# Performance work log

Hardware: AMD Instinct MI355X
Metric: run time of the kernel (lower is better)

## Reference

```python
import jax, jax.numpy as jnp
import numpy as np
import math

B, P, N, DM, H, DK, DH, DF = 2, 12, 170, 64, 8, 8, 32, 256
SQ = math.sqrt(DK)

def _ln(x, g, b):
    m = jnp.mean(x, -1, keepdims=True)
    v = jnp.var(x, -1, keepdims=True)
    return (x - m) / jnp.sqrt(v + 1e-5) * g + b

def _nozero_softmax(s):
    # faithful to nozero_softmax: mask = (s != 0), max over full row, +1e-5 in denom
    mask = (s != 0).astype(s.dtype)
    e = jnp.exp(s - jnp.max(s, -1, keepdims=True)) * mask
    return e / (jnp.sum(e, -1, keepdims=True) + 1e-5)

def _meta(c, w1, b1, w2, b2):
    # MetaLearner: [B,P,N,DM] -> [3,B,P,N,H,DK,DM]
    h = jax.nn.relu(c @ w1 + b1) @ w2 + b2
    h = h.reshape(c.shape[:3] + (3, H, DK, DM))
    return jnp.moveaxis(h, 3, 0)

def _mhlin(W, x):
    # multihead_linear_transform: per-position meta weight applied to x
    return jnp.einsum('bpnhkd,bpnd->bpnhk', W, x)

def _gdc(data, W1, W2):
    # Gated_Dynamic_Connection (noGC=False). data: [G,B,P,N,C]
    d = jnp.moveaxis(data, 0, 3)  # [B,P,N,G,C]
    a = jnp.einsum('bpngc,gcd->bpngd', d, W1)
    s = jax.nn.softmax(jax.nn.relu(jnp.einsum('bpngc,gcd->bpngd', d, W2)), axis=3)
    return jnp.sum(a * s, axis=3)  # [B,P,N,DM]

def _swish_gate(x, out, wg, bg, wo, bo):
    h = (x @ wg + bg) * out
    return (h * jax.nn.sigmoid(h)) @ wo + bo

def _spatial(Q, K, V, T):
    # adjacency-masked spatial attention. Dense-masked form is exactly the
    # scatter-into-zeros buffer of the original: zero where T==0, QK/sqrt(dk) on edges.
    s = jnp.einsum('bpihk,bpjhk->bphij', Q, K) / SQ
    Tb = T if T.ndim == 2 else T[:, :, None]  # adaptive graph [B,P,1,N,N]
    s = s * (Tb != 0)
    alpha = _nozero_softmax(s) * Tb
    return jnp.einsum('bphij,bpjhk->hbpik', alpha, V)  # [H,B,P,N,DK]

def _temporal(Q, K, V):
    s = jnp.einsum('bqnhk,bpnhk->bnhqp', Q, K) / SQ
    alpha = jax.nn.softmax(s, -1)
    return jnp.einsum('bnhqp,bpnhk->hbqnk', alpha, V)  # [H,B,P,N,DK]

def _retnet(Q, K, V, D):
    # multihead_temporal_regnet with g=1 leading dim folded in
    r = jnp.einsum('bqnhk,bpnhk->bnhqp', Q, K) / SQ
    r = r * D  # D: [H,P,P] causal decay
    rs = jnp.maximum(jnp.abs(jnp.sum(r, -1, keepdims=True)), 1.0)
    r = r / rs
    return jnp.einsum('bnhqp,bpnhk->hbqnk', r, V)  # [H,B,P,N,DK]

def _forward(x, c_x, enc, T, A, D, mr_w1, mr_b1, mr_w2, mr_b2, ms0_w1, ms0_b1, ms0_w2, ms0_b2, ms1_w1, ms1_b1, ms1_w2, ms1_b2, gr_W1, gr_W2, gs0_W1, gs0_W2, gs1_W1, gs1_W2, g2_W1, g2_W2, ge_W1, ge_W2, swr_wg, swr_bg, swr_wo, swr_bo, sws_wg, sws_bg, sws_wo, sws_bo, swe_wg, swe_bg, swe_wo, swe_bo, lnr_g, lnr_b, lns_g, lns_b, lne_g, lne_b, lnf_g, lnf_b, wq, wk, wv, f_w1, f_b1, f_w2, f_b2):
    # 1) RetNet-style temporal self retention (meta-learned QKV)
    W = _meta(c_x, mr_w1, mr_b1, mr_w2, mr_b2)
    o = _gdc(_retnet(_mhlin(W[0], x), _mhlin(W[1], x), _mhlin(W[2], x), D), gr_W1, gr_W2)
    o = _swish_gate(x, o, swr_wg, swr_bg, swr_wo, swr_bo)
    x1 = _ln(o + x, lnr_g, lnr_b)
    # 2) Spatial self attention: predefined graph + adaptive graph branches
    W0 = _meta(c_x, ms0_w1, ms0_b1, ms0_w2, ms0_b2)
    o0 = _gdc(_spatial(_mhlin(W0[0], x1), _mhlin(W0[1], x1), _mhlin(W0[2], x1), T), gs0_W1, gs0_W2)
    W1m = _meta(c_x, ms1_w1, ms1_b1, ms1_w2, ms1_b2)
    o1 = _gdc(_spatial(_mhlin(W1m[0], x1), _mhlin(W1m[1], x1), _mhlin(W1m[2], x1), A), gs1_W1, gs1_W2)
    o = _gdc(jnp.stack([o0, o1], 0), g2_W1, g2_W2)
    o = _swish_gate(x1, o, sws_wg, sws_bg, sws_wo, sws_bo)
    x2 = _ln(o + x1, lns_g, lns_b)
    # 3) Temporal encoder-decoder attention
    q = (x2 @ wq).reshape(B, P, N, H, DK)
    k = (enc @ wk).reshape(B, P, N, H, DK)
    v = (enc @ wv).reshape(B, P, N, H, DK)
    o = _gdc(_temporal(q, k, v), ge_W1, ge_W2)
    o = _swish_gate(x2, o, swe_wg, swe_bg, swe_wo, swe_bo)
    x3 = _ln(o + x2, lne_g, lne_b)
    # 4) FFN
    o = jax.nn.relu(x3 @ f_w1 + f_b1) @ f_w2 + f_b2
    return _ln(o + x3, lnf_g, lnf_b)


def setup_inputs() -> dict:
    key = jax.random.key(0)
    ks = iter(jax.random.split(key, 100))
    def rn(shape, s=0.05):
        return (jax.random.normal(next(ks), shape) * s).astype(jnp.float32)
    inp = {}
    inp['x'] = jax.random.normal(next(ks), (B, P, N, DM), jnp.float32)
    inp['c_x'] = jax.random.normal(next(ks), (B, P, N, DM), jnp.float32)
    inp['enc'] = jax.random.normal(next(ks), (B, P, N, DM), jnp.float32)
    mT = jax.random.uniform(next(ks), (N, N)) < 0.1
    inp['T'] = (jax.random.uniform(next(ks), (N, N)) * mT).astype(jnp.float32)
    mA = jax.random.uniform(next(ks), (B, P, N, N)) < 0.05
    inp['A'] = (jax.random.uniform(next(ks), (B, P, N, N)) * mA).astype(jnp.float32)
    q = np.arange(P)
    gam = 1.0 - 2.0 ** (-5.0 - np.arange(H))
    Dm = np.where(q[:, None] >= q[None, :], gam[:, None, None] ** (q[:, None] - q[None, :]), 0.0)
    inp['D'] = jnp.asarray(Dm, jnp.float32)  # [H,P,P]
    for p in ['mr', 'ms0', 'ms1']:
        inp[p + '_w1'] = rn((DM, DH)); inp[p + '_b1'] = jnp.zeros((DH,), jnp.float32)
        inp[p + '_w2'] = rn((DH, 3 * H * DK * DM)); inp[p + '_b2'] = jnp.zeros((3 * H * DK * DM,), jnp.float32)
    for p in ['gr', 'gs0', 'gs1', 'ge']:
        inp[p + '_W1'] = rn((H, DK, DM)); inp[p + '_W2'] = rn((H, DK, DM))
    inp['g2_W1'] = rn((2, DM, DM)); inp['g2_W2'] = rn((2, DM, DM))
    for p in ['swr', 'sws', 'swe']:
        inp[p + '_wg'] = rn((DM, DM)); inp[p + '_bg'] = jnp.zeros((DM,), jnp.float32)
        inp[p + '_wo'] = rn((DM, DM)); inp[p + '_bo'] = jnp.zeros((DM,), jnp.float32)
    for p in ['lnr', 'lns', 'lne', 'lnf']:
        inp[p + '_g'] = jnp.ones((DM,), jnp.float32); inp[p + '_b'] = jnp.zeros((DM,), jnp.float32)
    inp['wq'] = rn((DM, DM)); inp['wk'] = rn((DM, DM)); inp['wv'] = rn((DM, DM))
    inp['f_w1'] = rn((DM, DF)); inp['f_b1'] = jnp.zeros((DF,), jnp.float32)
    inp['f_w2'] = rn((DF, DM)); inp['f_b2'] = jnp.zeros((DM,), jnp.float32)
    return inp


def reference(x, c_x, enc, T, A, D, mr_w1, mr_b1, mr_w2, mr_b2, ms0_w1, ms0_b1, ms0_w2, ms0_b2, ms1_w1, ms1_b1, ms1_w2, ms1_b2, gr_W1, gr_W2, gs0_W1, gs0_W2, gs1_W1, gs1_W2, g2_W1, g2_W2, ge_W1, ge_W2, swr_wg, swr_bg, swr_wo, swr_bo, sws_wg, sws_bg, sws_wo, sws_bo, swe_wg, swe_bg, swe_wo, swe_bo, lnr_g, lnr_b, lns_g, lns_b, lne_g, lne_b, lnf_g, lnf_b, wq, wk, wv, f_w1, f_b1, f_w2, f_b2):
    return _forward(x, c_x, enc, T, A, D, mr_w1, mr_b1, mr_w2, mr_b2, ms0_w1, ms0_b1, ms0_w2, ms0_b2, ms1_w1, ms1_b1, ms1_w2, ms1_b2, gr_W1, gr_W2, gs0_W1, gs0_W2, gs1_W1, gs1_W2, g2_W1, g2_W2, ge_W1, ge_W2, swr_wg, swr_bg, swr_wo, swr_bo, sws_wg, sws_bg, sws_wo, sws_bo, swe_wg, swe_bg, swe_wo, swe_bo, lnr_g, lnr_b, lns_g, lns_b, lne_g, lne_b, lnf_g, lnf_b, wq, wk, wv, f_w1, f_b1, f_w2, f_b2)
```

## Files before the change

kernel.cpp:

```cpp
#include <hip/hip_runtime.h>
#include <hip/hip_bf16.h>
#include <math.h>

namespace {

constexpr int B_ = 2, P_ = 12, N_ = 170, DM_ = 64, H_ = 8, DK_ = 8, DH_ = 32, DF_ = 256;
constexpr int T_ = B_ * P_ * N_;
constexpr float SQRT_DK = 2.8284271247461903f;

constexpr int NG_ = 12;
constexpr int NC_ = 66;
constexpr int WFRAG_G = NG_ * NC_ * 64 * 8;

typedef __attribute__((ext_vector_type(4))) short short4v;
typedef __attribute__((ext_vector_type(8))) short short8v;
typedef __attribute__((ext_vector_type(4))) float float4v;

__device__ __forceinline__ unsigned short f2bf(float x) {
    union { float f; unsigned int u; } c; c.f = x;
    unsigned int r = (c.u + 0x7FFFu + ((c.u >> 16) & 1u)) >> 16;
    return (unsigned short)r;
}

__global__ void k_hr3(const float* __restrict__ c_x,
                      const float* __restrict__ w1a, const float* __restrict__ b1a,
                      const float* __restrict__ w1b, const float* __restrict__ b1b,
                      const float* __restrict__ w1c, const float* __restrict__ b1c,
                      float* __restrict__ hra, float* __restrict__ hrb,
                      float* __restrict__ hrc) {
    int z = blockIdx.y;
    const float* w1 = z == 0 ? w1a : (z == 1 ? w1b : w1c);
    const float* b1 = z == 0 ? b1a : (z == 1 ? b1b : b1c);
    float* hr = z == 0 ? hra : (z == 1 ? hrb : hrc);
    int idx = blockIdx.x * 256 + threadIdx.x;
    if (idx >= T_ * DH_) return;
    int t = idx / DH_, j = idx % DH_;
    float acc = b1[j];
    const float* cx = c_x + t * DM_;
    #pragma unroll
    for (int d = 0; d < DM_; ++d) acc += cx[d] * w1[d * DH_ + j];
    hr[idx] = fmaxf(acc, 0.f);
}

__global__ void k_wconv(const float* __restrict__ w2a, const float* __restrict__ b2a,
                        const float* __restrict__ w2b, const float* __restrict__ b2b,
                        const float* __restrict__ w2c, const float* __restrict__ b2c,
                        unsigned short* __restrict__ Wfrag) {
    int idx = blockIdx.x * 256 + threadIdx.x;
    if (idx >= 3 * NG_ * NC_ * 64) return;
    int lane = idx & 63;
    int c = (idx >> 6) % NC_;
    int ng = (idx >> 6) / NC_ % NG_;
    int g = idx / (64 * NC_ * NG_);
    const float* w2 = g == 0 ? w2a : (g == 1 ? w2b : w2c);
    const float* b2 = g == 0 ? b2a : (g == 1 ? b2b : b2c);
    int m = ng * 16 + (lane & 15);
    int u = c >> 1;
    int d0 = (c & 1) * 32 + (lane >> 4) * 8;
    const float* src = (u < DH_) ? (w2 + u * 12288 + m * 64 + d0) : (b2 + m * 64 + d0);
    short8v o;
    #pragma unroll
    for (int j = 0; j < 8; ++j) o[j] = (short)f2bf(src[j]);
    *(short8v*)(Wfrag + (size_t)idx * 8) = o;
}

__global__ __launch_bounds__(256) void k_meta_gemm2(
    const float* __restrict__ hr0, const float* __restrict__ hr1,
    const float* __restrict__ xin,
    const unsigned short* __restrict__ Wf0, const unsigned short* __restrict__ Wf1,
    float* __restrict__ out0, float* __restrict__ out1) {
    const int bz = blockIdx.z;
    const float* hr = bz ? hr1 : hr0;
    const unsigned short* Wf = bz ? Wf1 : Wf0;
    float* out = bz ? out1 : out0;

    const int tid = threadIdx.x;
    const int wv = tid >> 6, lane = tid & 63;
    const int l15 = lane & 15, quad = lane >> 4;
    const int g16 = blockIdx.x * 4 + wv;
    if (g16 >= 255) return;
    const int t = g16 * 16 + l15;
    const int nb = blockIdx.y;

    const float* xp = xin + t * 64 + quad * 8;
    float4v xa = *(const float4v*)(xp);
    float4v xb = *(const float4v*)(xp + 4);
    float4v xc = *(const float4v*)(xp + 32);
    float4v xd = *(const float4v*)(xp + 36);
    float xr[16] = {xa.x, xa.y, xa.z, xa.w, xb.x, xb.y, xb.z, xb.w,
                    xc.x, xc.y, xc.z, xc.w, xd.x, xd.y, xd.z, xd.w};

    const float* hrp = hr + t * 32;
    float4v acc[4] = {{0.f,0.f,0.f,0.f},{0.f,0.f,0.f,0.f},
                      {0.f,0.f,0.f,0.f},{0.f,0.f,0.f,0.f}};

    const unsigned short* wb = Wf + ((size_t)(nb * 4) * NC_ * 64 + lane) * 8;
    const size_t qstride = (size_t)NC_ * 64 * 8;
    const size_t cstride = 64 * 8;

    for (int u = 0; u < 33; ++u) {
        float hrv = (u < DH_) ? hrp[u] : 1.0f;
        short8v a0, a1;
        #pragma unroll
        for (int j = 0; j < 8; ++j) {
            a0[j] = (short)f2bf(hrv * xr[j]);
            a1[j] = (short)f2bf(hrv * xr[8 + j]);
        }
        const unsigned short* wc = wb + (size_t)(2 * u) * cstride;
        #pragma unroll
        for (int q = 0; q < 4; ++q) {
            short8v b0 = *(const short8v*)(wc + q * qstride);
            short8v b1 = *(const short8v*)(wc + q * qstride + cstride);
            acc[q] = __builtin_amdgcn_mfma_f32_16x16x32_bf16(a0, b0, acc[q], 0, 0, 0);
            acc[q] = __builtin_amdgcn_mfma_f32_16x16x32_bf16(a1, b1, acc[q], 0, 0, 0);
        }
    }

    #pragma unroll
    for (int q = 0; q < 4; ++q) {
        #pragma unroll
        for (int r = 0; r < 4; ++r) {
            int tt = g16 * 16 + quad * 4 + r;
            out[tt * 192 + nb * 64 + q * 16 + l15] = acc[q][r];
        }
    }
}

__global__ __launch_bounds__(256) void k_retnet(const float* __restrict__ qkv,
                                                const float* __restrict__ Dm,
                                                float* __restrict__ att) {
    const int bn = blockIdx.x;
    const int b = bn / N_, n = bn % N_;
    __shared__ float S[12][192];
    __shared__ float Ds[8 * 145];
    const int tid = threadIdx.x;
    for (int e = tid; e < 12 * 192; e += 256) {
        int p = e / 192, c = e % 192;
        S[p][c] = qkv[((size_t)((b * P_ + p) * N_ + n)) * 192 + c];
    }
    for (int e = tid; e < 1152; e += 256) {
        Ds[(e / 144) * 145 + (e % 144)] = Dm[e];
    }
    __syncthreads();
    const int qq = tid >> 6;
    const int lane = tid & 63;
    const int h = lane >> 3, k = lane & 7;
    for (int q = qq; q < P_; q += 4) {
        float Qv = S[q][h * 8 + k];
        float r[P_];
        float rsum = 0.f;
        #pragma unroll
        for (int p = 0; p < P_; ++p) {
            float prod = Qv * S[p][64 + h * 8 + k];
            prod += __shfl_xor(prod, 1, 64);
            prod += __shfl_xor(prod, 2, 64);
            prod += __shfl_xor(prod, 4, 64);
            float s = (prod / SQRT_DK) * Ds[h * 145 + q * 12 + p];
            r[p] = s; rsum += s;
        }
        float rs = fmaxf(fabsf(rsum), 1.0f);
        float acc = 0.f;
        #pragma unroll
        for (int p = 0; p < P_; ++p) acc += (r[p] / rs) * S[p][128 + h * 8 + k];
        att[((size_t)((b * P_ + q) * N_ + n)) * 64 + lane] = acc;
    }
}

__global__ __launch_bounds__(256) void k_temporal(const float* __restrict__ qkv,
                                                  float* __restrict__ att) {
    const int bn = blockIdx.x;
    const int b = bn / N_, n = bn % N_;
    __shared__ float S[12][192];
    const int tid = threadIdx.x;
    for (int e = tid; e < 12 * 192; e += 256) {
        int p = e / 192, c = e % 192;
        S[p][c] = qkv[((size_t)((b * P_ + p) * N_ + n)) * 192 + c];
    }
    __syncthreads();
    const int qq = tid >> 6;
    const int lane = tid & 63;
    const int h = lane >> 3, k = lane & 7;
    for (int q = qq; q < P_; q += 4) {
        float Qv = S[q][h * 8 + k];
        float s[P_];
        float mx = -1e30f;
        #pragma unroll
        for (int p = 0; p < P_; ++p) {
            float prod = Qv * S[p][64 + h * 8 + k];
            prod += __shfl_xor(prod, 1, 64);
            prod += __shfl_xor(prod, 2, 64);
            prod += __shfl_xor(prod, 4, 64);
            float v = prod / SQRT_DK;
            s[p] = v; mx = fmaxf(mx, v);
        }
        float den = 0.f, acc = 0.f;
        #pragma unroll
        for (int p = 0; p < P_; ++p) {
            float e = expf(s[p] - mx);
            den += e;
            acc += e * S[p][128 + h * 8 + k];
        }
        att[((size_t)((b * P_ + q) * N_ + n)) * 64 + lane] = acc / den;
    }
}

__global__ __launch_bounds__(256) void k_spatial_sparse(
    const float* __restrict__ qkvA, const float* __restrict__ qkvB,
    const float* __restrict__ Tm, const float* __restrict__ Am,
    float* __restrict__ attA, float* __restrict__ attB) {
    const int bp = blockIdx.y;
    const int g = blockIdx.z;
    const float* qkv = g ? qkvB : qkvA;
    float* att = g ? attB : attA;

    __shared__ int2 elist[4][176];

    const int tid = threadIdx.x;
    const int wv = tid >> 6, lane = tid & 63;
    const int i = blockIdx.x * 4 + wv;
    if (i >= N_) return;

    int2* el = elist[wv];
    const float* Trow = g ? (Am + (size_t)(bp * N_ + i) * N_) : (Tm + (size_t)i * N_);
    int nnz = 0;
    #pragma unroll
    for (int c = 0; c < 3; ++c) {
        int j = c * 64 + lane;
        float w = (j < N_) ? Trow[j] : 0.f;
        unsigned long long m = __ballot(w != 0.f);
        if (w != 0.f) {
            int pos = nnz + (int)__popcll(m & ((1ull << lane) - 1ull));
            el[pos] = make_int2(j, __float_as_int(w));
        }
        nnz += (int)__popcll(m);
    }

    const float q = qkv[(size_t)(bp * N_ + i) * 192 + lane];
    float m = 0.f;
    float den = 0.f, acc = 0.f;
    int e = 0;
    for (; e + 1 < nnz; e += 2) {
        int2 e0 = el[e], e1 = el[e + 1];
        const float* r0 = qkv + (size_t)(bp * N_ + e0.x) * 192;
        const float* r1 = qkv + (size_t)(bp * N_ + e1.x) * 192;
        float k0 = r0[64 + lane], v0 = r0[128 + lane];
        float k1 = r1[64 + lane], v1 = r1[128 + lane];
        float p0 = q * k0, p1 = q * k1;
        p0 += __shfl_xor(p0, 1, 64); p1 += __shfl_xor(p1, 1, 64);
        p0 += __shfl_xor(p0, 2, 64); p1 += __shfl_xor(p1, 2, 64);
        p0 += __shfl_xor(p0, 4, 64); p1 += __shfl_xor(p1, 4, 64);
        float s0 = p0 / SQRT_DK, s1 = p1 / SQRT_DK;
        float mn = fmaxf(m, fmaxf(s0, s1));
        float cs = expf(m - mn);
        float x0 = (s0 != 0.f) ? expf(s0 - mn) : 0.f;
        float x1 = (s1 != 0.f) ? expf(s1 - mn) : 0.f;
        den = den * cs + x0 + x1;
        acc = acc * cs + x0 * __int_as_float(e0.y) * v0
                       + x1 * __int_as_float(e1.y) * v1;
        m = mn;
    }
    if (e < nnz) {
        int2 e0 = el[e];
        const float* r0 = qkv + (size_t)(bp * N_ + e0.x) * 192;
        float k0 = r0[64 + lane], v0 = r0[128 + lane];
        float p0 = q * k0;
        p0 += __shfl_xor(p0, 1, 64);
        p0 += __shfl_xor(p0, 2, 64);
        p0 += __shfl_xor(p0, 4, 64);
        float s0 = p0 / SQRT_DK;
        float mn = fmaxf(m, s0);
        float cs = expf(m - mn);
        float x0 = (s0 != 0.f) ? expf(s0 - mn) : 0.f;
        den = den * cs + x0;
        acc = acc * cs + x0 * __int_as_float(e0.y) * v0;
    }

    att[(size_t)(bp * N_ + i) * 64 + lane] = acc / (den + 1e-5f);
}

__device__ __forceinline__ float gdc8(const float* dv, const float* W1,
                                      const float* W2, int dm) {
    float a[8], s[8];
    #pragma unroll
    for (int g = 0; g < 8; ++g) {
        float aa = 0.f, ss = 0.f;
        #pragma unroll
        for (int c = 0; c < 8; ++c) {
            float d = dv[g * 8 + c];
            aa += d * W1[(g * 8 + c) * 64 + dm];
            ss += d * W2[(g * 8 + c) * 64 + dm];
        }
        a[g] = aa; s[g] = fmaxf(ss, 0.f);
    }
    float mx = s[0];
    #pragma unroll
    for (int g = 1; g < 8; ++g) mx = fmaxf(mx, s[g]);
    float den = 0.f, o = 0.f;
    #pragma unroll
    for (int g = 0; g < 8; ++g) { float e = expf(s[g] - mx); den += e; o += a[g] * e; }
    return o / den;
}

__device__ __forceinline__ float ln_out(float r, int dm, const float* g, const float* b) {
    float m = r, m2 = r * r;
    #pragma unroll
    for (int off = 32; off; off >>= 1) { m += __shfl_xor(m, off, 64); m2 += __shfl_xor(m2, off, 64); }
    m *= (1.f / 64.f); m2 *= (1.f / 64.f);
    float var = m2 - m * m;
    return (r - m) * rsqrtf(var + 1e-5f) * g[dm] + b[dm];
}

__global__ __launch_bounds__(64) void k_gsl(const float* __restrict__ att, const float* __restrict__ xin,
    const float* W1, const float* W2,
    const float* wg, const float* bg,
    const float* wo, const float* bo,
    const float* lng, const float* lnb, float* __restrict__ xout) {
    int t = blockIdx.x, dm = threadIdx.x;
    __shared__ float dv[64], xv[64], swv[64];
    dv[dm] = att[t * 64 + dm];
    xv[dm] = xin[t * 64 + dm];
    __syncthreads();
    float o = gdc8(dv, W1, W2, dm);
    float hg = bg[dm];
    #pragma unroll
    for (int d = 0; d < 64; ++d) hg += xv[d] * wg[d * 64 + dm];
    hg *= o;
    swv[dm] = hg / (1.f + expf(-hg));
    __syncthreads();
    float ov = bo[dm];
    #pragma unroll
    for (int d = 0; d < 64; ++d) ov += swv[d] * wo[d * 64 + dm];
    float r = ov + xv[dm];
    xout[t * 64 + dm] = ln_out(r, dm, lng, lnb);
}

__global__ __launch_bounds__(64) void k_spatial_fuse(
    const float* __restrict__ att0, const float* __restrict__ att1, const float* __restrict__ x1,
    const float* gs0_W1, const float* gs0_W2,
    const float* gs1_W1, const float* gs1_W2,
    const float* g2_W1, const float* g2_W2,
    const float* wg, const float* bg,
    const float* wo, const float* bo,
    const float* lng, const float* lnb, float* __restrict__ xout) {
    int t = blockIdx.x, dm = threadIdx.x;
    __shared__ float d0[64], d1[64], o0s[64], o1s[64], xv[64], swv[64];
    d0[dm] = att0[t * 64 + dm];
    d1[dm] = att1[t * 64 + dm];
    xv[dm] = x1[t * 64 + dm];
    __syncthreads();
    o0s[dm] = gdc8(d0, gs0_W1, gs0_W2, dm);
    o1s[dm] = gdc8(d1, gs1_W1, gs1_W2, dm);
    __syncthreads();
    float a0 = 0.f, s0 = 0.f, a1 = 0.f, s1 = 0.f;
    #pragma unroll
    for (int c = 0; c < 64; ++c) {
        a0 += o0s[c] * g2_W1[c * 64 + dm];
        s0 += o0s[c] * g2_W2[c * 64 + dm];
        a1 += o1s[c] * g2_W1[(64 + c) * 64 + dm];
        s1 += o1s[c] * g2_W2[(64 + c) * 64 + dm];
    }
    s0 = fmaxf(s0, 0.f); s1 = fmaxf(s1, 0.f);
    float mx = fmaxf(s0, s1);
    float e0 = expf(s0 - mx), e1 = expf(s1 - mx);
    float o = (a0 * e0 + a1 * e1) / (e0 + e1);
    float hg = bg[dm];
    #pragma unroll
    for (int d = 0; d < 64; ++d) hg += xv[d] * wg[d * 64 + dm];
    hg *= o;
    swv[dm] = hg / (1.f + expf(-hg));
    __syncthreads();
    float ov = bo[dm];
    #pragma unroll
    for (int d = 0; d < 64; ++d) ov += swv[d] * wo[d * 64 + dm];
    float r = ov + xv[dm];
    xout[t * 64 + dm] = ln_out(r, dm, lng, lnb);
}

__global__ __launch_bounds__(64) void k_qkvproj(const float* __restrict__ x2,
    const float* __restrict__ enc,
    const float* wq, const float* wk, const float* wv,
    float* __restrict__ qkv) {
    int t = blockIdx.x, dm = threadIdx.x;
    __shared__ float xv[64], ev[64];
    xv[dm] = x2[t * 64 + dm];
    ev[dm] = enc[t * 64 + dm];
    __syncthreads();
    float aq = 0.f, ak = 0.f, av = 0.f;
    #pragma unroll
    for (int d = 0; d < 64; ++d) {
        aq += xv[d] * wq[d * 64 + dm];
        ak += ev[d] * wk[d * 64 + dm];
        av += ev[d] * wv[d * 64 + dm];
    }
    qkv[t * 192 + dm] = aq;
    qkv[t * 192 + 64 + dm] = ak;
    qkv[t * 192 + 128 + dm] = av;
}

__global__ __launch_bounds__(64) void k_ffn(const float* __restrict__ x3,
    const float* w1, const float* b1,
    const float* w2, const float* b2,
    const float* lng, const float* lnb,
    float* __restrict__ out) {
    int t = blockIdx.x, dm = threadIdx.x;
    __shared__ float xv[64], hv[256];
    xv[dm] = x3[t * 64 + dm];
    __syncthreads();
    #pragma unroll
    for (int e = 0; e < 4; ++e) {
        int j = e * 64 + dm;
        float a = b1[j];
        #pragma unroll
        for (int d = 0; d < 64; ++d) a += xv[d] * w1[d * 256 + j];
        hv[j] = fmaxf(a, 0.f);
    }
    __syncthreads();
    float a = b2[dm];
    for (int j = 0; j < 256; ++j) a += hv[j] * w2[j * 64 + dm];
    float r = a + xv[dm];
    out[t * 64 + dm] = ln_out(r, dm, lng, lnb);
}

}

extern "C" void kernel_launch(void* const* d_in, const int* in_sizes, int n_in,
                              void* d_out, int out_size, void* d_ws, size_t ws_size,
                              hipStream_t stream) {
    (void)in_sizes; (void)n_in; (void)out_size; (void)ws_size;
    const float* x    = (const float*)d_in[0];
    const float* c_x  = (const float*)d_in[1];
    const float* enc  = (const float*)d_in[2];
    const float* Tm   = (const float*)d_in[3];
    const float* Am   = (const float*)d_in[4];
    const float* Dm   = (const float*)d_in[5];
    const float* mr_w1 = (const float*)d_in[6];
    const float* mr_b1 = (const float*)d_in[7];
    const float* mr_w2 = (const float*)d_in[8];
    const float* mr_b2 = (const float*)d_in[9];
    const float* ms0_w1 = (const float*)d_in[10];
    const float* ms0_b1 = (const float*)d_in[11];
    const float* ms0_w2 = (const float*)d_in[12];
    const float* ms0_b2 = (const float*)d_in[13];
    const float* ms1_w1 = (const float*)d_in[14];
    const float* ms1_b1 = (const float*)d_in[15];
    const float* ms1_w2 = (const float*)d_in[16];
    const float* ms1_b2 = (const float*)d_in[17];
    const float* gr_W1 = (const float*)d_in[18];
    const float* gr_W2 = (const float*)d_in[19];
    const float* gs0_W1 = (const float*)d_in[20];
    const float* gs0_W2 = (const float*)d_in[21];
    const float* gs1_W1 = (const float*)d_in[22];
    const float* gs1_W2 = (const float*)d_in[23];
    const float* g2_W1 = (const float*)d_in[24];
    const float* g2_W2 = (const float*)d_in[25];
    const float* ge_W1 = (const float*)d_in[26];
    const float* ge_W2 = (const float*)d_in[27];
    const float* swr_wg = (const float*)d_in[28];
    const float* swr_bg = (const float*)d_in[29];
    const float* swr_wo = (const float*)d_in[30];
    const float* swr_bo = (const float*)d_in[31];
    const float* sws_wg = (const float*)d_in[32];
    const float* sws_bg = (const float*)d_in[33];
    const float* sws_wo = (const float*)d_in[34];
    const float* sws_bo = (const float*)d_in[35];
    const float* swe_wg = (const float*)d_in[36];
    const float* swe_bg = (const float*)d_in[37];
    const float* swe_wo = (const float*)d_in[38];
    const float* swe_bo = (const float*)d_in[39];
    const float* lnr_g = (const float*)d_in[40];
    const float* lnr_b = (const float*)d_in[41];
    const float* lns_g = (const float*)d_in[42];
    const float* lns_b = (const float*)d_in[43];
    const float* lne_g = (const float*)d_in[44];
    const float* lne_b = (const float*)d_in[45];
    const float* lnf_g = (const float*)d_in[46];
    const float* lnf_b = (const float*)d_in[47];
    const float* wq = (const float*)d_in[48];
    const float* wk = (const float*)d_in[49];
    const float* wv = (const float*)d_in[50];
    const float* f_w1 = (const float*)d_in[51];
    const float* f_b1 = (const float*)d_in[52];
    const float* f_w2 = (const float*)d_in[53];
    const float* f_b2 = (const float*)d_in[54];

    float* ws   = (float*)d_ws;
    float* hr   = ws;
    float* hr2  = hr   + T_ * DH_;
    float* qkva = hr2  + T_ * DH_;
    float* qkvb = qkva + T_ * 192;
    float* atta = qkvb + T_ * 192;
    float* attb = atta + T_ * DM_;
    float* x1f  = attb + T_ * DM_;
    float* x2f  = x1f  + T_ * DM_;
    float* x3f  = x2f  + T_ * DM_;
    unsigned short* Wfrag = (unsigned short*)(x3f + T_ * DM_);
    float* hr_r = attb;

    k_wconv<<<(3 * NG_ * NC_ * 64 + 255) / 256, 256, 0, stream>>>(
        mr_w2, mr_b2, ms0_w2, ms0_b2, ms1_w2, ms1_b2, Wfrag);

    k_hr3<<<dim3(510, 3), 256, 0, stream>>>(c_x, mr_w1, mr_b1, ms0_w1, ms0_b1,
                                            ms1_w1, ms1_b1, hr_r, hr, hr2);

    k_meta_gemm2<<<dim3(64, 3, 1), 256, 0, stream>>>(
        hr_r, hr_r, x, Wfrag, Wfrag, qkva, qkva);
    k_retnet<<<B_ * N_, 256, 0, stream>>>(qkva, Dm, atta);
    k_gsl<<<T_, 64, 0, stream>>>(atta, x, gr_W1, gr_W2, swr_wg, swr_bg, swr_wo, swr_bo,
                                 lnr_g, lnr_b, x1f);

    k_meta_gemm2<<<dim3(64, 3, 2), 256, 0, stream>>>(
        hr, hr2, x1f, Wfrag + WFRAG_G, Wfrag + 2 * WFRAG_G, qkva, qkvb);
    k_spatial_sparse<<<dim3((N_ + 3) / 4, B_ * P_, 2), 256, 0, stream>>>(
        qkva, qkvb, Tm, Am, atta, attb);
    k_spatial_fuse<<<T_, 64, 0, stream>>>(atta, attb, x1f, gs0_W1, gs0_W2, gs1_W1, gs1_W2,
                                          g2_W1, g2_W2, sws_wg, sws_bg, sws_wo, sws_bo,
                                          lns_g, lns_b, x2f);

    k_qkvproj<<<T_, 64, 0, stream>>>(x2f, enc, wq, wk, wv, qkva);
    k_temporal<<<B_ * N_, 256, 0, stream>>>(qkva, atta);
    k_gsl<<<T_, 64, 0, stream>>>(atta, x2f, ge_W1, ge_W2, swe_wg, swe_bg, swe_wo, swe_bo,
                                 lne_g, lne_b, x3f);

    k_ffn<<<T_, 64, 0, stream>>>(x3f, f_w1, f_b1, f_w2, f_b2, lnf_g, lnf_b, (float*)d_out);
}
```

Baseline: 324.7 us.

## Fuse attention kernels with gated-dynamic-connection/swish/layernorm epilogues and merge prep kernels

Merges the weight conversion and hidden-layer prep kernels into one launch. Fuses retnet attention with its GDC/swish-gate/layernorm stage, spatial sparse attention (both graphs) with its fuse stage, and QKV projection plus temporal attention plus its gated stage into single kernels. The meta GEMM loop now loads hr as float4 and peels the bias step. This cuts launch count and intermediate global round-trips, but the fused epilogues run serialized per wave inside blocks with fewer blocks overall (340 for temporal/retnet), which may lower parallelism.

```diff
diff --git a/kernel.cpp b/kernel.cpp
--- a/kernel.cpp
+++ b/kernel.cpp
@@ -22,46 +22,46 @@
     return (unsigned short)r;
 }
 
-__global__ void k_hr3(const float* __restrict__ c_x,
+__global__ void k_pre(const float* __restrict__ c_x,
                       const float* __restrict__ w1a, const float* __restrict__ b1a,
                       const float* __restrict__ w1b, const float* __restrict__ b1b,
                       const float* __restrict__ w1c, const float* __restrict__ b1c,
+                      const float* __restrict__ w2a, const float* __restrict__ b2a,
+                      const float* __restrict__ w2b, const float* __restrict__ b2b,
+                      const float* __restrict__ w2c, const float* __restrict__ b2c,
                       float* __restrict__ hra, float* __restrict__ hrb,
-                      float* __restrict__ hrc) {
-    int z = blockIdx.y;
-    const float* w1 = z == 0 ? w1a : (z == 1 ? w1b : w1c);
-    const float* b1 = z == 0 ? b1a : (z == 1 ? b1b : b1c);
-    float* hr = z == 0 ? hra : (z == 1 ? hrb : hrc);
-    int idx = blockIdx.x * 256 + threadIdx.x;
-    if (idx >= T_ * DH_) return;
-    int t = idx / DH_, j = idx % DH_;
-    float acc = b1[j];
-    const float* cx = c_x + t * DM_;
-    #pragma unroll
-    for (int d = 0; d < DM_; ++d) acc += cx[d] * w1[d * DH_ + j];
-    hr[idx] = fmaxf(acc, 0.f);
-}
-
-__global__ void k_wconv(const float* __restrict__ w2a, const float* __restrict__ b2a,
-                        const float* __restrict__ w2b, const float* __restrict__ b2b,
-                        const float* __restrict__ w2c, const float* __restrict__ b2c,
-                        unsigned short* __restrict__ Wfrag) {
-    int idx = blockIdx.x * 256 + threadIdx.x;
-    if (idx >= 3 * NG_ * NC_ * 64) return;
-    int lane = idx & 63;
-    int c = (idx >> 6) % NC_;
-    int ng = (idx >> 6) / NC_ % NG_;
-    int g = idx / (64 * NC_ * NG_);
-    const float* w2 = g == 0 ? w2a : (g == 1 ? w2b : w2c);
-    const float* b2 = g == 0 ? b2a : (g == 1 ? b2b : b2c);
-    int m = ng * 16 + (lane & 15);
-    int u = c >> 1;
-    int d0 = (c & 1) * 32 + (lane >> 4) * 8;
-    const float* src = (u < DH_) ? (w2 + u * 12288 + m * 64 + d0) : (b2 + m * 64 + d0);
-    short8v o;
-    #pragma unroll
-    for (int j = 0; j < 8; ++j) o[j] = (short)f2bf(src[j]);
-    *(short8v*)(Wfrag + (size_t)idx * 8) = o;
+                      float* __restrict__ hrc, unsigned short* __restrict__ Wfrag) {
+    if (blockIdx.y == 0) {
+        int idx = blockIdx.x * 256 + threadIdx.x;
+        if (idx >= 3 * NG_ * NC_ * 64) return;
+        int lane = idx & 63;
+        int c = (idx >> 6) % NC_;
+        int ng = (idx >> 6) / NC_ % NG_;
+        int g = idx / (64 * NC_ * NG_);
+        const float* w2 = g == 0 ? w2a : (g == 1 ? w2b : w2c);
+        const float* b2 = g == 0 ? b2a : (g == 1 ? b2b : b2c);
+        int m = ng * 16 + (lane & 15);
+        int u = c >> 1;
+        int d0 = (c & 1) * 32 + (lane >> 4) * 8;
+        const float* src = (u < DH_) ? (w2 + u * 12288 + m * 64 + d0) : (b2 + m * 64 + d0);
+        short8v o;
+        #pragma unroll
+        for (int j = 0; j < 8; ++j) o[j] = (short)f2bf(src[j]);
+        *(short8v*)(Wfrag + (size_t)idx * 8) = o;
+    } else {
+        int z = blockIdx.y - 1;
+        const float* w1 = z == 0 ? w1a : (z == 1 ? w1b : w1c);
+        const float* b1 = z == 0 ? b1a : (z == 1 ? b1b : b1c);
+        float* hr = z == 0 ? hra : (z == 1 ? hrb : hrc);
+        int idx = blockIdx.x * 256 + threadIdx.x;
+        if (idx >= T_ * DH_) return;
+        int t = idx / DH_, j = idx % DH_;
+        float acc = b1[j];
+        const float* cx = c_x + t * DM_;
+        #pragma unroll
+        for (int d = 0; d < DM_; ++d) acc += cx[d] * w1[d * DH_ + j];
+        hr[idx] = fmaxf(acc, 0.f);
+    }
 }
 
 __global__ __launch_bounds__(256) void k_meta_gemm2(
@@ -98,15 +98,37 @@
     const size_t qstride = (size_t)NC_ * 64 * 8;
     const size_t cstride = 64 * 8;
 
-    for (int u = 0; u < 33; ++u) {
-        float hrv = (u < DH_) ? hrp[u] : 1.0f;
+    #pragma unroll 1
+    for (int u0 = 0; u0 < 32; u0 += 4) {
+        float4v h4 = *(const float4v*)(hrp + u0);
+        float hv4[4] = {h4.x, h4.y, h4.z, h4.w};
+        #pragma unroll
+        for (int du = 0; du < 4; ++du) {
+            float hrv = hv4[du];
+            short8v a0, a1;
+            #pragma unroll
+            for (int j = 0; j < 8; ++j) {
+                a0[j] = (short)f2bf(hrv * xr[j]);
+                a1[j] = (short)f2bf(hrv * xr[8 + j]);
+            }
+            const unsigned short* wc = wb + (size_t)(2 * (u0 + du)) * cstride;
+            #pragma unroll
+            for (int q = 0; q < 4; ++q) {
+                short8v b0 = *(const short8v*)(wc + q * qstride);
+                short8v b1 = *(const short8v*)(wc + q * qstride + cstride);
+                acc[q] = __builtin_amdgcn_mfma_f32_16x16x32_bf16(a0, b0, acc[q], 0, 0, 0);
+                acc[q] = __builtin_amdgcn_mfma_f32_16x16x32_bf16(a1, b1, acc[q], 0, 0, 0);
+            }
+        }
+    }
+    {
         short8v a0, a1;
         #pragma unroll
         for (int j = 0; j < 8; ++j) {
-            a0[j] = (short)f2bf(hrv * xr[j]);
-            a1[j] = (short)f2bf(hrv * xr[8 + j]);
-        }
-        const unsigned short* wc = wb + (size_t)(2 * u) * cstride;
+            a0[j] = (short)f2bf(xr[j]);
+            a1[j] = (short)f2bf(xr[8 + j]);
+        }
+        const unsigned short* wc = wb + (size_t)64 * cstride;
         #pragma unroll
         for (int q = 0; q < 4; ++q) {
             short8v b0 = *(const short8v*)(wc + q * qstride);
@@ -126,13 +148,50 @@
     }
 }
 
-__global__ __launch_bounds__(256) void k_retnet(const float* __restrict__ qkv,
-                                                const float* __restrict__ Dm,
-                                                float* __restrict__ att) {
+__device__ __forceinline__ float gdc8(const float* dv, const float* W1,
+                                      const float* W2, int dm) {
+    float a[8], s[8];
+    #pragma unroll
+    for (int g = 0; g < 8; ++g) {
+        float aa = 0.f, ss = 0.f;
+        #pragma unroll
+        for (int c = 0; c < 8; ++c) {
+            float d = dv[g * 8 + c];
+            aa += d * W1[(g * 8 + c) * 64 + dm];
+            ss += d * W2[(g * 8 + c) * 64 + dm];
+        }
+        a[g] = aa; s[g] = fmaxf(ss, 0.f);
+    }
+    float mx = s[0];
+    #pragma unroll
+    for (int g = 1; g < 8; ++g) mx = fmaxf(mx, s[g]);
+    float den = 0.f, o = 0.f;
+    #pragma unroll
+    for (int g = 0; g < 8; ++g) { float e = expf(s[g] - mx); den += e; o += a[g] * e; }
+    return o / den;
+}
+
+__device__ __forceinline__ float ln_out(float r, int dm, const float* g, const float* b) {
+    float m = r, m2 = r * r;
+    #pragma unroll
+    for (int off = 32; off; off >>= 1) { m += __shfl_xor(m, off, 64); m2 += __shfl_xor(m2, off, 64); }
+    m *= (1.f / 64.f); m2 *= (1.f / 64.f);
+    float var = m2 - m * m;
+    return (r - m) * rsqrtf(var + 1e-5f) * g[dm] + b[dm];
+}
+
+__global__ __launch_bounds__(256) void k_retnet_gsl(
+    const float* __restrict__ qkv, const float* __restrict__ Dm,
+    const float* __restrict__ xin,
+    const float* W1, const float* W2,
+    const float* wg, const float* bg, const float* wo, const float* bo,
+    const float* lng, const float* lnb,
+    float* __restrict__ x1f) {
     const int bn = blockIdx.x;
     const int b = bn / N_, n = bn % N_;
     __shared__ float S[12][192];
     __shared__ float Ds[8 * 145];
+    __shared__ float dvr[4][64], xvr[4][64], swb[4][64];
     const int tid = threadIdx.x;
     for (int e = tid; e < 12 * 192; e += 256) {
         int p = e / 192, c = e % 192;
@@ -142,10 +201,10 @@
         Ds[(e / 144) * 145 + (e % 144)] = Dm[e];
     }
     __syncthreads();
-    const int qq = tid >> 6;
+    const int wv = tid >> 6;
     const int lane = tid & 63;
     const int h = lane >> 3, k = lane & 7;
-    for (int q = qq; q < P_; q += 4) {
+    for (int q = wv; q < P_; q += 4) {
         float Qv = S[q][h * 8 + k];
         float r[P_];
         float rsum = 0.f;
@@ -162,25 +221,64 @@
         float acc = 0.f;
         #pragma unroll
         for (int p = 0; p < P_; ++p) acc += (r[p] / rs) * S[p][128 + h * 8 + k];
-        att[((size_t)((b * P_ + q) * N_ + n)) * 64 + lane] = acc;
-    }
-}
-
-__global__ __launch_bounds__(256) void k_temporal(const float* __restrict__ qkv,
-                                                  float* __restrict__ att) {
+
+        const size_t t64 = (size_t)((b * P_ + q) * N_ + n) * 64;
+        dvr[wv][lane] = acc;
+        xvr[wv][lane] = xin[t64 + lane];
+        __syncthreads();
+        float o = gdc8(dvr[wv], W1, W2, lane);
+        float hg = bg[lane];
+        #pragma unroll
+        for (int d = 0; d < 64; ++d) hg += xvr[wv][d] * wg[d * 64 + lane];
+        hg *= o;
+        swb[wv][lane] = hg / (1.f + expf(-hg));
+        __syncthreads();
+        float ov = bo[lane];
+        #pragma unroll
+        for (int d = 0; d < 64; ++d) ov += swb[wv][d] * wo[d * 64 + lane];
+        float rr = ov + xvr[wv][lane];
+        x1f[t64 + lane] = ln_out(rr, lane, lng, lnb);
+        __syncthreads();
+    }
+}
+
+__global__ __launch_bounds__(256) void k_temporal_full(
+    const float* __restrict__ x2f, const float* __restrict__ enc,
+    const float* __restrict__ wqm, const float* __restrict__ wkm,
+    const float* __restrict__ wvm,
+    const float* W1, const float* W2,
+    const float* wg, const float* bg, const float* wo, const float* bo,
+    const float* lng, const float* lnb,
+    float* __restrict__ x3f) {
     const int bn = blockIdx.x;
     const int b = bn / N_, n = bn % N_;
+    __shared__ float Sx[12][64], Se[12][64];
     __shared__ float S[12][192];
+    __shared__ float dvr[4][64], swb[4][64];
     const int tid = threadIdx.x;
-    for (int e = tid; e < 12 * 192; e += 256) {
-        int p = e / 192, c = e % 192;
-        S[p][c] = qkv[((size_t)((b * P_ + p) * N_ + n)) * 192 + c];
-    }
-    __syncthreads();
-    const int qq = tid >> 6;
+    for (int e = tid; e < 768; e += 256) {
+        int p = e >> 6, c = e & 63;
+        size_t t64 = (size_t)((b * P_ + p) * N_ + n) * 64;
+        Sx[p][c] = x2f[t64 + c];
+        Se[p][c] = enc[t64 + c];
+    }
+    __syncthreads();
+    #pragma unroll
+    for (int it = 0; it < 9; ++it) {
+        int e = it * 256 + tid;
+        int p = e / 192, j = e % 192;
+        const float* src = (j < 64) ? Sx[p] : Se[p];
+        const float* wm = (j < 64) ? (wqm + j) : (j < 128 ? (wkm + j - 64) : (wvm + j - 128));
+        float a = 0.f;
+        #pragma unroll
+        for (int d = 0; d < 64; ++d) a += src[d] * wm[d * 64];
+        S[p][j] = a;
+    }
+    __syncthreads();
+    const int wv = tid >> 6;
     const int lane = tid & 63;
     const int h = lane >> 3, k = lane & 7;
-    for (int q = qq; q < P_; q += 4) {
+    for (int q = wv; q < P_; q += 4) {
         float Qv = S[q][h * 8 + k];
         float s[P_];
         float mx = -1e30f;
@@ -200,201 +298,142 @@
             den += e;
             acc += e * S[p][128 + h * 8 + k];
         }
-        att[((size_t)((b * P_ + q) * N_ + n)) * 64 + lane] = acc / den;
-    }
-}
-
-__global__ __launch_bounds__(256) void k_spatial_sparse(
+        const size_t t64 = (size_t)((b * P_ + q) * N_ + n) * 64;
+        dvr[wv][lane] = acc / den;
+        __syncthreads();
+        float o = gdc8(dvr[wv], W1, W2, lane);
+        float hg = bg[lane];
+        #pragma unroll
+        for (int d = 0; d < 64; ++d) hg += Sx[q][d] * wg[d * 64 + lane];
+        hg *= o;
+        swb[wv][lane] = hg / (1.f + expf(-hg));
+        __syncthreads();
+        float ov = bo[lane];
+        #pragma unroll
+        for (int d = 0; d < 64; ++d) ov += swb[wv][d] * wo[d * 64 + lane];
+        float rr = ov + Sx[q][lane];
+        x3f[t64 + lane] = ln_out(rr, lane, lng, lnb);
+        __syncthreads();
+    }
+}
+
+__global__ __launch_bounds__(256) void k_spatial_all(
     const float* __restrict__ qkvA, const float* __restrict__ qkvB,
     const float* __restrict__ Tm, const float* __restrict__ Am,
-    float* __restrict__ attA, float* __restrict__ attB) {
+    const float* __restrict__ x1f,
+    const float* gs0_W1, const float* gs0_W2,
+    const float* gs1_W1, const float* gs1_W2,
+    const float* g2_W1, const float* g2_W2,
+    const float* wg, const float* bg, const float* wo, const float* bo,
+    const float* lng, const float* lnb,
+    float* __restrict__ x2f) {
     const int bp = blockIdx.y;
-    const int g = blockIdx.z;
-    const float* qkv = g ? qkvB : qkvA;
-    float* att = g ? attB : attA;
-
-    __shared__ int2 elist[4][176];
-
     const int tid = threadIdx.x;
     const int wv = tid >> 6, lane = tid & 63;
     const int i = blockIdx.x * 4 + wv;
-    if (i >= N_) return;
+    const bool active = (i < N_);
+
+    __shared__ int2 elist[4][176];
+    __shared__ float d0r[4][64], d1r[4][64], o0r[4][64], o1r[4][64], xvr[4][64], swb[4][64];
 
     int2* el = elist[wv];
-    const float* Trow = g ? (Am + (size_t)(bp * N_ + i) * N_) : (Tm + (size_t)i * N_);
-    int nnz = 0;
-    #pragma unroll
-    for (int c = 0; c < 3; ++c) {
-        int j = c * 64 + lane;
-        float w = (j < N_) ? Trow[j] : 0.f;
-        unsigned long long m = __ballot(w != 0.f);
-        if (w != 0.f) {
-            int pos = nnz + (int)__popcll(m & ((1ull << lane) - 1ull));
-            el[pos] = make_int2(j, __float_as_int(w));
-        }
-        nnz += (int)__popcll(m);
-    }
-
-    const float q = qkv[(size_t)(bp * N_ + i) * 192 + lane];
-    float m = 0.f;
-    float den = 0.f, acc = 0.f;
-    int e = 0;
-    for (; e + 1 < nnz; e += 2) {
-        int2 e0 = el[e], e1 = el[e + 1];
-        const float* r0 = qkv + (size_t)(bp * N_ + e0.x) * 192;
-        const float* r1 = qkv + (size_t)(bp * N_ + e1.x) * 192;
-        float k0 = r0[64 + lane], v0 = r0[128 + lane];
-        float k1 = r1[64 + lane], v1 = r1[128 + lane];
-        float p0 = q * k0, p1 = q * k1;
-        p0 += __shfl_xor(p0, 1, 64); p1 += __shfl_xor(p1, 1, 64);
-        p0 += __shfl_xor(p0, 2, 64); p1 += __shfl_xor(p1, 2, 64);
-        p0 += __shfl_xor(p0, 4, 64); p1 += __shfl_xor(p1, 4, 64);
-        float s0 = p0 / SQRT_DK, s1 = p1 / SQRT_DK;
-        float mn = fmaxf(m, fmaxf(s0, s1));
-        float cs = expf(m - mn);
-        float x0 = (s0 != 0.f) ? expf(s0 - mn) : 0.f;
-        float x1 = (s1 != 0.f) ? expf(s1 - mn) : 0.f;
-        den = den * cs + x0 + x1;
-        acc = acc * cs + x0 * __int_as_float(e0.y) * v0
-                       + x1 * __int_as_float(e1.y) * v1;
-        m = mn;
-    }
-    if (e < nnz) {
-        int2 e0 = el[e];
-        const float* r0 = qkv + (size_t)(bp * N_ + e0.x) * 192;
-        float k0 = r0[64 + lane], v0 = r0[128 + lane];
-        float p0 = q * k0;
-        p0 += __shfl_xor(p0, 1, 64);
-        p0 += __shfl_xor(p0, 2, 64);
-        p0 += __shfl_xor(p0, 4, 64);
-        float s0 = p0 / SQRT_DK;
-        float mn = fmaxf(m, s0);
-        float cs = expf(m - mn);
-        float x0 = (s0 != 0.f) ? expf(s0 - mn) : 0.f;
-        den = den * cs + x0;
-        acc = acc * cs + x0 * __int_as_float(e0.y) * v0;
-    }
-
-    att[(size_t)(bp * N_ + i) * 64 + lane] = acc / (den + 1e-5f);
-}
-
-__device__ __forceinline__ float gdc8(const float* dv, const float* W1,
-                                      const float* W2, int dm) {
-    float a[8], s[8];
-    #pragma unroll
-    for (int g = 0; g < 8; ++g) {
-        float aa = 0.f, ss = 0.f;
-        #pragma unroll
-        for (int c = 0; c < 8; ++c) {
-            float d = dv[g * 8 + c];
-            aa += d * W1[(g * 8 + c) * 64 + dm];
-            ss += d * W2[(g * 8 + c) * 64 + dm];
-        }
-        a[g] = aa; s[g] = fmaxf(ss, 0.f);
-    }
-    float mx = s[0];
-    #pragma unroll
-    for (int g = 1; g < 8; ++g) mx = fmaxf(mx, s[g]);
-    float den = 0.f, o = 0.f;
-    #pragma unroll
-    for (int g = 0; g < 8; ++g) { float e = expf(s[g] - mx); den += e; o += a[g] * e; }
-    return o / den;
-}
-
-__device__ __forceinline__ float ln_out(float r, int dm, const float* g, const float* b) {
-    float m = r, m2 = r * r;
-    #pragma unroll
-    for (int off = 32; off; off >>= 1) { m += __shfl_xor(m, off, 64); m2 += __shfl_xor(m2, off, 64); }
-    m *= (1.f / 64.f); m2 *= (1.f / 64.f);
-    float var = m2 - m * m;
-    return (r - m) * rsqrtf(var + 1e-5f) * g[dm] + b[dm];
-}
-
-__global__ __launch_bounds__(64) void k_gsl(const float* __restrict__ att, const float* __restrict__ xin,
-    const float* W1, const float* W2,
-    const float* wg, const float* bg,
-    const float* wo, const float* bo,
-    const float* lng, const float* lnb, float* __restrict__ xout) {
-    int t = blockIdx.x, dm = threadIdx.x;
-    __shared__ float dv[64], xv[64], swv[64];
-    dv[dm] = att[t * 64 + dm];
-    xv[dm] = xin[t * 64 + dm];
-    __syncthreads();
-    float o = gdc8(dv, W1, W2, dm);
-    float hg = bg[dm];
-    #pragma unroll
-    for (int d = 0; d < 64; ++d) hg += xv[d] * wg[d * 64 + dm];
-    hg *= o;
-    swv[dm] = hg / (1.f + expf(-hg));
-    __syncthreads();
-    float ov = bo[dm];
-    #pragma unroll
-    for (int d = 0; d < 64; ++d) ov += swv[d] * wo[d * 64 + dm];
-    float r = ov + xv[dm];
-    xout[t * 64 + dm] = ln_out(r, dm, lng, lnb);
-}
-
-__global__ __launch_bounds__(64) void k_spatial_fuse(
-    const float* __restrict__ att0, const float* __restrict__ att1, const float* __restrict__ x1,
-    const float* gs0_W1, const float* gs0_W2,
-    const float* gs1_W1, const float* gs1_W2,
-    const float* g2_W1, const float* g2_W2,
-    const float* wg, const float* bg,
-    const float* wo, const float* bo,
-    const float* lng, const float* lnb, float* __restrict__ xout) {
-    int t = blockIdx.x, dm = threadIdx.x;
-    __shared__ float d0[64], d1[64], o0s[64], o1s[64], xv[64], swv[64];
-    d0[dm] = att0[t * 64 + dm];
-    d1[dm] = att1[t * 64 + dm];
-    xv[dm] = x1[t * 64 + dm];
-    __syncthreads();
-    o0s[dm] = gdc8(d0, gs0_W1, gs0_W2, dm);
-    o1s[dm] = gdc8(d1, gs1_W1, gs1_W2, dm);
+    float att[2] = {0.f, 0.f};
+    #pragma unroll
+    for (int g = 0; g < 2; ++g) {
+        const float* qkv = g ? qkvB : qkvA;
+        int nnz = 0;
+        if (active) {
+            const float* Trow = g ? (Am + (size_t)(bp * N_ + i) * N_) : (Tm + (size_t)i * N_);
+            #pragma unroll
+            for (int c = 0; c < 3; ++c) {
+                int j = c * 64 + lane;
+                float w = (j < N_) ? Trow[j] : 0.f;
+                unsigned long long mm = __ballot(w != 0.f);
+                if (w != 0.f) {
+                    int pos = nnz + (int)__popcll(mm & ((1ull << lane) - 1ull));
+                    el[pos] = make_int2(j, __float_as_int(w));
+                }
+                nnz += (int)__popcll(mm);
+            }
+        }
+        const float qv = active ? qkv[(size_t)(bp * N_ + i) * 192 + lane] : 0.f;
+        float m = 0.f;
+        float den = 0.f, acc = 0.f;
+        int e = 0;
+        for (; e + 1 < nnz; e += 2) {
+            int2 e0 = el[e], e1 = el[e + 1];
+            const float* r0 = qkv + (size_t)(bp * N_ + e0.x) * 192;
+            const float* r1 = qkv + (size_t)(bp * N_ + e1.x) * 192;
+            float k0 = r0[64 + lane], v0 = r0[128 + lane];
+            float k1 = r1[64 + lane], v1 = r1[128 + lane];
+            float p0 = qv * k0, p1 = qv * k1;
+            p0 += __shfl_xor(p0, 1, 64); p1 += __shfl_xor(p1, 1, 64);
+            p0 += __shfl_xor(p0, 2, 64); p1 += __shfl_xor(p1, 2, 64);
+            p0 += __shfl_xor(p0, 4, 64); p1 += __shfl_xor(p1, 4, 64);
+            float s0 = p0 / SQRT_DK, s1 = p1 / SQRT_DK;
+            float mn = fmaxf(m, fmaxf(s0, s1));
+            float cs = expf(m - mn);
+            float x0 = (s0 != 0.f) ? expf(s0 - mn) : 0.f;
+            float x1 = (s1 != 0.f) ? expf(s1 - mn) : 0.f;
+            den = den * cs + x0 + x1;
+            acc = acc * cs + x0 * __int_as_float(e0.y) * v0
+                           + x1 * __int_as_float(e1.y) * v1;
+            m = mn;
+        }
+        if (e < nnz) {
+            int2 e0 = el[e];
+            const float* r0 = qkv + (size_t)(bp * N_ + e0.x) * 192;
+            float k0 = r0[64 + lane], v0 = r0[128 + lane];
+            float p0 = qv * k0;
+            p0 += __shfl_xor(p0, 1, 64);
+            p0 += __shfl_xor(p0, 2, 64);
+            p0 += __shfl_xor(p0, 4, 64);
+            float s0 = p0 / SQRT_DK;
+            float mn = fmaxf(m, s0);
+            float cs = expf(m - mn);
+            float x0 = (s0 != 0.f) ? expf(s0 - mn) : 0.f;
+            den = den * cs + x0;
+            acc = acc * cs + x0 * __int_as_float(e0.y) * v0;
+        }
+        att[g] = acc / (den + 1e-5f);
+    }
+
+    if (active) {
+        d0r[wv][lane] = att[0];
+        d1r[wv][lane] = att[1];
+        xvr[wv][lane] = x1f[(size_t)(bp * N_ + i) * 64 + lane];
+    } else {
+        d0r[wv][lane] = 0.f; d1r[wv][lane] = 0.f; xvr[wv][lane] = 0.f;
+    }
+    __syncthreads();
+    o0r[wv][lane] = gdc8(d0r[wv], gs0_W1, gs0_W2, lane);
+    o1r[wv][lane] = gdc8(d1r[wv], gs1_W1, gs1_W2, lane);
     __syncthreads();
     float a0 = 0.f, s0 = 0.f, a1 = 0.f, s1 = 0.f;
     #pragma unroll
     for (int c = 0; c < 64; ++c) {
-        a0 += o0s[c] * g2_W1[c * 64 + dm];
-        s0 += o0s[c] * g2_W2[c * 64 + dm];
-        a1 += o1s[c] * g2_W1[(64 + c) * 64 + dm];
-        s1 += o1s[c] * g2_W2[(64 + c) * 64 + dm];
+        float v0 = o0r[wv][c], v1 = o1r[wv][c];
+        a0 += v0 * g2_W1[c * 64 + lane];
+        s0 += v0 * g2_W2[c * 64 + lane];
+        a1 += v1 * g2_W1[(64 + c) * 64 + lane];
+        s1 += v1 * g2_W2[(64 + c) * 64 + lane];
     }
     s0 = fmaxf(s0, 0.f); s1 = fmaxf(s1, 0.f);
     float mx = fmaxf(s0, s1);
     float e0 = expf(s0 - mx), e1 = expf(s1 - mx);
     float o = (a0 * e0 + a1 * e1) / (e0 + e1);
-    float hg = bg[dm];
-    #pragma unroll
-    for (int d = 0; d < 64; ++d) hg += xv[d] * wg[d * 64 + dm];
+    float hg = bg[lane];
+    #pragma unroll
+    for (int d = 0; d < 64; ++d) hg += xvr[wv][d] * wg[d * 64 + lane];
     hg *= o;
-    swv[dm] = hg / (1.f + expf(-hg));
-    __syncthreads();
-    float ov = bo[dm];
-    #pragma unroll
-    for (int d = 0; d < 64; ++d) ov += swv[d] * wo[d * 64 + dm];
-    float r = ov + xv[dm];
-    xout[t * 64 + dm] = ln_out(r, dm, lng, lnb);
-}
-
-__global__ __launch_bounds__(64) void k_qkvproj(const float* __restrict__ x2,
-    const float* __restrict__ enc,
-    const float* wq, const float* wk, const float* wv,
-    float* __restrict__ qkv) {
-    int t = blockIdx.x, dm = threadIdx.x;
-    __shared__ float xv[64], ev[64];
-    xv[dm] = x2[t * 64 + dm];
-    ev[dm] = enc[t * 64 + dm];
-    __syncthreads();
-    float aq = 0.f, ak = 0.f, av = 0.f;
-    #pragma unroll
-    for (int d = 0; d < 64; ++d) {
-        aq += xv[d] * wq[d * 64 + dm];
-        ak += ev[d] * wk[d * 64 + dm];
-        av += ev[d] * wv[d * 64 + dm];
-    }
-    qkv[t * 192 + dm] = aq;
-    qkv[t * 192 + 64 + dm] = ak;
-    qkv[t * 192 + 128 + dm] = av;
+    swb[wv][lane] = hg / (1.f + expf(-hg));
+    __syncthreads();
+    float ov = bo[lane];
+    #pragma unroll
+    for (int d = 0; d < 64; ++d) ov += swb[wv][d] * wo[d * 64 + lane];
+    float rr = ov + xvr[wv][lane];
+    float res = ln_out(rr, lane, lng, lnb);
+    if (active) x2f[(size_t)(bp * N_ + i) * 64 + lane] = res;
 }
 
 __global__ __launch_bounds__(64) void k_ffn(const float* __restrict__ x3,
@@ -496,30 +535,24 @@
     unsigned short* Wfrag = (unsigned short*)(x3f + T_ * DM_);
     float* hr_r = attb;
 
-    k_wconv<<<(3 * NG_ * NC_ * 64 + 255) / 256, 256, 0, stream>>>(
-        mr_w2, mr_b2, ms0_w2, ms0_b2, ms1_w2, ms1_b2, Wfrag);
-
-    k_hr3<<<dim3(510, 3), 256, 0, stream>>>(c_x, mr_w1, mr_b1, ms0_w1, ms0_b1,
-                                            ms1_w1, ms1_b1, hr_r, hr, hr2);
+    k_pre<<<dim3(594, 4), 256, 0, stream>>>(
+        c_x, mr_w1, mr_b1, ms0_w1, ms0_b1, ms1_w1, ms1_b1,
+        mr_w2, mr_b2, ms0_w2, ms0_b2, ms1_w2, ms1_b2,
+        hr_r, hr, hr2, Wfrag);
 
     k_meta_gemm2<<<dim3(64, 3, 1), 256, 0, stream>>>(
         hr_r, hr_r, x, Wfrag, Wfrag, qkva, qkva);
-    k_retnet<<<B_ * N_, 256, 0, stream>>>(qkva, Dm, atta);
-    k_gsl<<<T_, 64, 0, stream>>>(atta, x, gr_W1, gr_W2, swr_wg, swr_bg, swr_wo, swr_bo,
-                                 lnr_g, lnr_b, x1f);
+    k_retnet_gsl<<<B_ * N_, 256, 0, stream>>>(qkva, Dm, x, gr_W1, gr_W2,
+        swr_wg, swr_bg, swr_wo, swr_bo, lnr_g, lnr_b, x1f);
 
     k_meta_gemm2<<<dim3(64, 3, 2), 256, 0, stream>>>(
         hr, hr2, x1f, Wfrag + WFRAG_G, Wfrag + 2 * WFRAG_G, qkva, qkvb);
-    k_spatial_sparse<<<dim3((N_ + 3) / 4, B_ * P_, 2), 256, 0, stream>>>(
-        qkva, qkvb, Tm, Am, atta, attb);
-    k_spatial_fuse<<<T_, 64, 0, stream>>>(atta, attb, x1f, gs0_W1, gs0_W2, gs1_W1, gs1_W2,
-                                          g2_W1, g2_W2, sws_wg, sws_bg, sws_wo, sws_bo,
-                                          lns_g, lns_b, x2f);
-
-    k_qkvproj<<<T_, 64, 0, stream>>>(x2f, enc, wq, wk, wv, qkva);
-    k_temporal<<<B_ * N_, 256, 0, stream>>>(qkva, atta);
-    k_gsl<<<T_, 64, 0, stream>>>(atta, x2f, ge_W1, ge_W2, swe_wg, swe_bg, swe_wo, swe_bo,
-                                 lne_g, lne_b, x3f);
+    k_spatial_all<<<dim3((N_ + 3) / 4, B_ * P_), 256, 0, stream>>>(
+        qkva, qkvb, Tm, Am, x1f, gs0_W1, gs0_W2, gs1_W1, gs1_W2,
+        g2_W1, g2_W2, sws_wg, sws_bg, sws_wo, sws_bo, lns_g, lns_b, x2f);
+
+    k_temporal_full<<<B_ * N_, 256, 0, stream>>>(x2f, enc, wq, wk, wv,
+        ge_W1, ge_W2, swe_wg, swe_bg, swe_wo, swe_bo, lne_g, lne_b, x3f);
 
     k_ffn<<<T_, 64, 0, stream>>>(x3f, f_w1, f_b1, f_w2, f_b2, lnf_g, lnf_b, (float*)d_out);
 }
```

Measured after the change: 599.1 us. 1.85x slower.
